# Performance work log

Hardware: AMD Instinct MI355X
Metric: run time of the kernel (lower is better)

Reference implementation:

```python
import jax, jax.numpy as jnp
import numpy as np

HIDDEN = 1024
FFN = 3584
NUM_EXPERTS = 8
TOP_K = 2
B, S = 2, 1024


def setup_inputs() -> dict:
    key = jax.random.key(0)
    k0, k1, k2, k3 = jax.random.split(key, 4)
    hidden_states = jax.random.normal(k0, (B, S, HIDDEN), dtype=jnp.float32)
    # torch Linear stores [out, in]; we keep gate as [E, H] (matches nn.Linear weight)
    gate_w = jax.random.normal(k1, (NUM_EXPERTS, HIDDEN), dtype=jnp.float32) * 0.02
    # GroupedLinear weights stored as [E, in, out] for direct x @ W per expert
    w_gate_up = jax.random.normal(k2, (NUM_EXPERTS, HIDDEN, 2 * FFN), dtype=jnp.float32) * 0.02
    w_down = jax.random.normal(k3, (NUM_EXPERTS, FFN, HIDDEN), dtype=jnp.float32) * 0.02
    return {"hidden_states": hidden_states, "gate_w": gate_w,
            "w_gate_up": w_gate_up, "w_down": w_down}


def reference(hidden_states, gate_w, w_gate_up, w_down):
    b, s, h = hidden_states.shape
    x = hidden_states.reshape(-1, h)                      # [T, H]
    T = x.shape[0]
    E = gate_w.shape[0]

    # Router: logits -> fp32 softmax -> top-k -> renormalize (Mixtral semantics)
    router_logits = x @ gate_w.T                          # [T, E]
    probs = jax.nn.softmax(router_logits.astype(jnp.float32), axis=-1)
    top_vals, top_idx = jax.lax.top_k(probs, TOP_K)       # [T, K]
    top_vals = top_vals / top_vals.sum(axis=-1, keepdims=True)
    top_vals = top_vals.astype(x.dtype)

    # Dense combine weights [T, E]: scatter top-k probs to expert slots.
    # Equivalent to permute -> grouped GEMM -> unpermute-with-probs.
    combine = jnp.zeros((T, E), dtype=x.dtype).at[
        jnp.arange(T)[:, None], top_idx].add(top_vals)

    out = jnp.zeros_like(x)
    for e in range(E):  # fixed small expert count
        gu = x @ w_gate_up[e]                             # [T, 2F]
        gate_proj, up_proj = jnp.split(gu, 2, axis=-1)
        act = jax.nn.silu(gate_proj) * up_proj            # [T, F]
        out = out + combine[:, e:e + 1] * (act @ w_down[e])

    return out.reshape(b, s, h), router_logits
```

## Files before the change

### kernel.cpp

```cpp
#include <hip/hip_runtime.h>
#include <hip/hip_bf16.h>
#include <stdint.h>

#define HIDDEN  1024
#define FFN     3584
#define NE      8
#define NTOK    2048
#define CAP     2048
#define OUT_ELEMS (NTOK * HIDDEN)

#define X_OFF   0u
#define CNT_OFF (4u*1024u*1024u)
#define TOK_OFF (CNT_OFF + 256u)
#define WGT_OFF (TOK_OFF + 65536u)
#define ACT_OFF (WGT_OFF + 65536u)

typedef __attribute__((ext_vector_type(8))) short short8;
typedef __attribute__((ext_vector_type(4))) float floatx4;

static __device__ __forceinline__ uint32_t f2bf(float f) {
  union { float f; uint32_t u; } v; v.f = f;
  return (v.u + 0x7FFFu + ((v.u >> 16) & 1u)) >> 16;
}
static __device__ __forceinline__ uint32_t pack2(float lo, float hi) {
  return f2bf(lo) | (f2bf(hi) << 16);
}
union S8U { uint4 u; short8 s; };
static __device__ __forceinline__ short8 as_short8(uint4 v) { S8U x; x.u = v; return x.s; }

__global__ __launch_bounds__(256) void moe_prep(float4* __restrict__ out4,
                                                int* __restrict__ cnt) {
  uint32_t i = blockIdx.x * 256u + threadIdx.x;
  out4[i] = make_float4(0.f, 0.f, 0.f, 0.f);
  if (blockIdx.x == 0 && threadIdx.x < NE) cnt[threadIdx.x] = 0;
}

__global__ __launch_bounds__(256) void moe_convert(const float4* __restrict__ x4,
                                                   uint4* __restrict__ xb) {
  uint32_t g = blockIdx.x * 256u + threadIdx.x;
  float4 a = x4[2u*g], b = x4[2u*g + 1u];
  xb[g] = make_uint4(pack2(a.x, a.y), pack2(a.z, a.w),
                     pack2(b.x, b.y), pack2(b.z, b.w));
}

__global__ __launch_bounds__(256) void moe_router(
    const float* __restrict__ x, const float* __restrict__ gw,
    float* __restrict__ logits, int* __restrict__ cnt,
    int* __restrict__ tok, float* __restrict__ wgt)
{
  const int t = blockIdx.x * 4 + (threadIdx.x >> 6);
  const int lane = threadIdx.x & 63;
  const float* xr = x + (size_t)t * HIDDEN;
  float a[NE];
#pragma unroll
  for (int e = 0; e < NE; ++e) a[e] = 0.f;
  for (int hh = 0; hh < HIDDEN / 64; ++hh) {
    float xv = xr[hh * 64 + lane];
#pragma unroll
    for (int e = 0; e < NE; ++e) a[e] += xv * gw[e * HIDDEN + hh * 64 + lane];
  }
#pragma unroll
  for (int off = 32; off > 0; off >>= 1) {
#pragma unroll
    for (int e = 0; e < NE; ++e) a[e] += __shfl_xor(a[e], off);
  }
  if (lane == 0) {
#pragma unroll
    for (int e = 0; e < NE; ++e) logits[t * NE + e] = a[e];
    int i0 = 0; float v0 = a[0];
#pragma unroll
    for (int e = 1; e < NE; ++e) if (a[e] > v0) { v0 = a[e]; i0 = e; }
    int i1 = (i0 == 0) ? 1 : 0; float v1 = a[i1];
#pragma unroll
    for (int e = 0; e < NE; ++e) if (e != i0 && a[e] > v1) { v1 = a[e]; i1 = e; }
    float w0 = 1.f / (1.f + __expf(v1 - v0));
    float w1 = 1.f - w0;
    int p0 = atomicAdd(&cnt[i0], 1); tok[i0 * CAP + p0] = t; wgt[i0 * CAP + p0] = w0;
    int p1 = atomicAdd(&cnt[i1], 1); tok[i1 * CAP + p1] = t; wgt[i1 * CAP + p1] = w1;
  }
}

__global__ __launch_bounds__(256) void moe_gateup(
    const uint4* __restrict__ xb, const float* __restrict__ wgu,
    const int* __restrict__ cnt, const int* __restrict__ tok,
    unsigned short* __restrict__ act)
{
  const int e  = blockIdx.z;
  const int m0 = blockIdx.y * 128;
  const int f0 = blockIdx.x * 64;
  const int cn = cnt[e];
  if (m0 >= cn) return;
  int basev = 0;
#pragma unroll
  for (int i = 0; i < NE; ++i) { int ci = cnt[i]; if (i < e) basev += ci; }

  __shared__ uint4    As[1024];
  __shared__ uint32_t Bs[4096];

  const int tid  = threadIdx.x;
  const int lane = tid & 63;
  const int w    = tid >> 6;
  const int wm   = w >> 1, wn = w & 1;
  const int q    = lane >> 4;
  const int c    = lane & 15;

  floatx4 acc[4][4];
#pragma unroll
  for (int i = 0; i < 4; ++i)
#pragma unroll
    for (int j = 0; j < 4; ++j) acc[i][j] = (floatx4){0.f, 0.f, 0.f, 0.f};

  const float* wB  = wgu + (size_t)e * HIDDEN * (2 * FFN);
  const int* tokE  = tok + e * CAP;

  for (int kt = 0; kt < HIDDEN / 64; ++kt) {
    const int k0 = kt * 64;
    __syncthreads();
#pragma unroll
    for (int it = 0; it < 4; ++it) {
      int cid = it * 256 + tid;
      int row = cid >> 3, c8 = cid & 7;
      int mrow = m0 + row; if (mrow >= cn) mrow = cn - 1;
      int tk = tokE[mrow];
      As[row * 8 + (c8 ^ (row & 7))] = xb[(size_t)tk * (HIDDEN / 8) + (k0 >> 3) + c8];
    }
#pragma unroll
    for (int it = 0; it < 4; ++it) {
      int mid = it * 256 + tid;
      int kp = mid >> 5;
      int n  = (mid & 31) * 4;
      int col = f0 + ((n >> 6) << 5) + (n & 31) + (((n >> 5) & 1) ? FFN : 0);
      const float* src = wB + (size_t)(k0 + 2 * kp) * (2 * FFN) + col;
      float4 r0 = *(const float4*)src;
      float4 r1 = *(const float4*)(src + 2 * FFN);
      int widx = kp * 128 + (n ^ (((kp >> 2) & 1) << 4));
      *(uint4*)&Bs[widx] = make_uint4(pack2(r0.x, r1.x), pack2(r0.y, r1.y),
                                      pack2(r0.z, r1.z), pack2(r0.w, r1.w));
    }
    __syncthreads();
#pragma unroll
    for (int ks = 0; ks < 2; ++ks) {
      short8 af[4];
#pragma unroll
      for (int i = 0; i < 4; ++i) {
        int row = wm * 64 + i * 16 + c;
        int kc8 = ks * 4 + q;
        af[i] = as_short8(As[row * 8 + (kc8 ^ (row & 7))]);
      }
      short8 bfr[4];
#pragma unroll
      for (int j = 0; j < 4; ++j) {
        int n  = wn * 64 + j * 16 + c;
        int kp = ks * 16 + q * 4;
        int nn = n ^ ((q & 1) << 4);
        bfr[j] = as_short8(make_uint4(Bs[(kp + 0) * 128 + nn], Bs[(kp + 1) * 128 + nn],
                                      Bs[(kp + 2) * 128 + nn], Bs[(kp + 3) * 128 + nn]));
      }
#pragma unroll
      for (int i = 0; i < 4; ++i)
#pragma unroll
        for (int j = 0; j < 4; ++j)
          acc[i][j] = __builtin_amdgcn_mfma_f32_16x16x32_bf16(af[i], bfr[j], acc[i][j], 0, 0, 0);
    }
  }

#pragma unroll
  for (int i = 0; i < 4; ++i) {
#pragma unroll
    for (int r = 0; r < 4; ++r) {
      int m = m0 + wm * 64 + i * 16 + q * 4 + r;
      if (m < cn) {
#pragma unroll
        for (int j = 0; j < 2; ++j) {
          float g = acc[i][j][r];
          float u = acc[i][j + 2][r];
          float a = (g / (1.f + __expf(-g))) * u;
          act[(size_t)(basev + m) * FFN + (f0 + wn * 32 + j * 16 + c)] = (unsigned short)f2bf(a);
        }
      }
    }
  }
}

__global__ __launch_bounds__(256) void moe_down(
    const uint4* __restrict__ actc, const float* __restrict__ wd,
    const int* __restrict__ cnt, const int* __restrict__ tok,
    const float* __restrict__ wgt, float* __restrict__ out)
{
  const int e  = blockIdx.z;
  const int m0 = blockIdx.y * 128;
  const int n0 = blockIdx.x * 128;
  const int cn = cnt[e];
  if (m0 >= cn) return;
  int basev = 0;
#pragma unroll
  for (int i = 0; i < NE; ++i) { int ci = cnt[i]; if (i < e) basev += ci; }

  __shared__ uint4    As[1024];
  __shared__ uint32_t Bs[4096];

  const int tid  = threadIdx.x;
  const int lane = tid & 63;
  const int w    = tid >> 6;
  const int wm   = w >> 1, wn = w & 1;
  const int q    = lane >> 4;
  const int c    = lane & 15;

  floatx4 acc[4][4];
#pragma unroll
  for (int i = 0; i < 4; ++i)
#pragma unroll
    for (int j = 0; j < 4; ++j) acc[i][j] = (floatx4){0.f, 0.f, 0.f, 0.f};

  const float* wB = wd + (size_t)e * FFN * HIDDEN;

  for (int kt = 0; kt < FFN / 64; ++kt) {
    const int k0 = kt * 64;
    __syncthreads();
#pragma unroll
    for (int it = 0; it < 4; ++it) {
      int cid = it * 256 + tid;
      int row = cid >> 3, c8 = cid & 7;
      int mrow = m0 + row; if (mrow >= cn) mrow = cn - 1;
      As[row * 8 + (c8 ^ (row & 7))] =
          actc[(size_t)(basev + mrow) * (FFN / 8) + (k0 >> 3) + c8];
    }
#pragma unroll
    for (int it = 0; it < 4; ++it) {
      int mid = it * 256 + tid;
      int kp = mid >> 5;
      int n  = (mid & 31) * 4;
      int col = n0 + n;
      const float* src = wB + (size_t)(k0 + 2 * kp) * HIDDEN + col;
      float4 r0 = *(const float4*)src;
      float4 r1 = *(const float4*)(src + HIDDEN);
      int widx = kp * 128 + (n ^ (((kp >> 2) & 1) << 4));
      *(uint4*)&Bs[widx] = make_uint4(pack2(r0.x, r1.x), pack2(r0.y, r1.y),
                                      pack2(r0.z, r1.z), pack2(r0.w, r1.w));
    }
    __syncthreads();
#pragma unroll
    for (int ks = 0; ks < 2; ++ks) {
      short8 af[4];
#pragma unroll
      for (int i = 0; i < 4; ++i) {
        int row = wm * 64 + i * 16 + c;
        int kc8 = ks * 4 + q;
        af[i] = as_short8(As[row * 8 + (kc8 ^ (row & 7))]);
      }
      short8 bfr[4];
#pragma unroll
      for (int j = 0; j < 4; ++j) {
        int n  = wn * 64 + j * 16 + c;
        int kp = ks * 16 + q * 4;
        int nn = n ^ ((q & 1) << 4);
        bfr[j] = as_short8(make_uint4(Bs[(kp + 0) * 128 + nn], Bs[(kp + 1) * 128 + nn],
                                      Bs[(kp + 2) * 128 + nn], Bs[(kp + 3) * 128 + nn]));
      }
#pragma unroll
      for (int i = 0; i < 4; ++i)
#pragma unroll
        for (int j = 0; j < 4; ++j)
          acc[i][j] = __builtin_amdgcn_mfma_f32_16x16x32_bf16(af[i], bfr[j], acc[i][j], 0, 0, 0);
    }
  }

#pragma unroll
  for (int i = 0; i < 4; ++i) {
#pragma unroll
    for (int r = 0; r < 4; ++r) {
      int m = m0 + wm * 64 + i * 16 + q * 4 + r;
      if (m < cn) {
        int   t  = tok[e * CAP + m];
        float wg = wgt[e * CAP + m];
        float* orow = out + (size_t)t * HIDDEN + n0 + wn * 64 + c;
#pragma unroll
        for (int j = 0; j < 4; ++j)
          atomicAdd(orow + j * 16, acc[i][j][r] * wg);
      }
    }
  }
}

extern "C" void kernel_launch(void* const* d_in, const int* in_sizes, int n_in,
                              void* d_out, int out_size, void* d_ws, size_t ws_size,
                              hipStream_t stream)
{
  (void)in_sizes; (void)n_in; (void)out_size; (void)ws_size;
  const float* x   = (const float*)d_in[0];
  const float* gw  = (const float*)d_in[1];
  const float* wgu = (const float*)d_in[2];
  const float* wd  = (const float*)d_in[3];
  float* out = (float*)d_out;
  char*  ws  = (char*)d_ws;

  uint4*          xb  = (uint4*)(ws + X_OFF);
  int*            cnt = (int*)(ws + CNT_OFF);
  int*            tok = (int*)(ws + TOK_OFF);
  float*          wgt = (float*)(ws + WGT_OFF);
  unsigned short* act = (unsigned short*)(ws + ACT_OFF);

  moe_prep<<<OUT_ELEMS / (256 * 4), 256, 0, stream>>>((float4*)out, cnt);
  moe_convert<<<(NTOK * HIDDEN) / (256 * 8), 256, 0, stream>>>((const float4*)x, xb);
  moe_router<<<NTOK / 4, 256, 0, stream>>>(x, gw, out + OUT_ELEMS, cnt, tok, wgt);
  moe_gateup<<<dim3(FFN / 64, 16, NE), 256, 0, stream>>>(xb, wgu, cnt, tok, act);
  moe_down<<<dim3(HIDDEN / 128, 16, NE), 256, 0, stream>>>((const uint4*)act, wd, cnt, tok, wgt, out);
}
```

Baseline: 630.8 us.

## Fuse bf16 convert into router, retile expert GEMMs with tall M tiles and split-K down

The separate x-to-bf16 conversion kernel is folded into the router, which now reads x as float4 and computes logits from registers. Both expert GEMMs switch to 512-thread blocks with 512-row M tiles and narrow 32/64-column N tiles over K=32 steps. The fp32 weight tiles are register-prefetched one step ahead and stored in small padded LDS buffers. The down projection is split four ways along K, with partial sums combined through the existing atomics. The aim is to stream each weight byte fewer times per expert and add more blocks to the down GEMM, at the cost of smaller K steps, more syncs per FLOP and more output atomics.

```diff
diff --git a/kernel.cpp b/kernel.cpp
--- a/kernel.cpp
+++ b/kernel.cpp
@@ -4,6 +4,7 @@
 
 #define HIDDEN  1024
 #define FFN     3584
+#define FFN2    7168
 #define NE      8
 #define NTOK    2048
 #define CAP     2048
@@ -35,29 +36,29 @@
   if (blockIdx.x == 0 && threadIdx.x < NE) cnt[threadIdx.x] = 0;
 }
 
-__global__ __launch_bounds__(256) void moe_convert(const float4* __restrict__ x4,
-                                                   uint4* __restrict__ xb) {
-  uint32_t g = blockIdx.x * 256u + threadIdx.x;
-  float4 a = x4[2u*g], b = x4[2u*g + 1u];
-  xb[g] = make_uint4(pack2(a.x, a.y), pack2(a.z, a.w),
-                     pack2(b.x, b.y), pack2(b.z, b.w));
-}
-
 __global__ __launch_bounds__(256) void moe_router(
-    const float* __restrict__ x, const float* __restrict__ gw,
+    const float4* __restrict__ x4, const float* __restrict__ gw,
     float* __restrict__ logits, int* __restrict__ cnt,
-    int* __restrict__ tok, float* __restrict__ wgt)
-{
-  const int t = blockIdx.x * 4 + (threadIdx.x >> 6);
+    int* __restrict__ tok, float* __restrict__ wgt, uint4* __restrict__ xb)
+{
+  const int w    = threadIdx.x >> 6;
   const int lane = threadIdx.x & 63;
-  const float* xr = x + (size_t)t * HIDDEN;
+  const int t    = blockIdx.x * 4 + w;
+  const float4* xr = x4 + (size_t)t * 256 + lane * 4;
+  float4 v0 = xr[0], v1 = xr[1], v2 = xr[2], v3 = xr[3];
+  xb[(size_t)t * 128 + lane * 2 + 0] =
+      make_uint4(pack2(v0.x, v0.y), pack2(v0.z, v0.w), pack2(v1.x, v1.y), pack2(v1.z, v1.w));
+  xb[(size_t)t * 128 + lane * 2 + 1] =
+      make_uint4(pack2(v2.x, v2.y), pack2(v2.z, v2.w), pack2(v3.x, v3.y), pack2(v3.z, v3.w));
   float a[NE];
 #pragma unroll
-  for (int e = 0; e < NE; ++e) a[e] = 0.f;
-  for (int hh = 0; hh < HIDDEN / 64; ++hh) {
-    float xv = xr[hh * 64 + lane];
-#pragma unroll
-    for (int e = 0; e < NE; ++e) a[e] += xv * gw[e * HIDDEN + hh * 64 + lane];
+  for (int e = 0; e < NE; ++e) {
+    const float4* g4 = (const float4*)(gw + e * HIDDEN) + lane * 4;
+    float4 g0 = g4[0], g1 = g4[1], g2 = g4[2], g3 = g4[3];
+    a[e] = v0.x*g0.x + v0.y*g0.y + v0.z*g0.z + v0.w*g0.w
+         + v1.x*g1.x + v1.y*g1.y + v1.z*g1.z + v1.w*g1.w
+         + v2.x*g2.x + v2.y*g2.y + v2.z*g2.z + v2.w*g2.w
+         + v3.x*g3.x + v3.y*g3.y + v3.z*g3.z + v3.w*g3.w;
   }
 #pragma unroll
   for (int off = 32; off > 0; off >>= 1) {
@@ -67,145 +68,147 @@
   if (lane == 0) {
 #pragma unroll
     for (int e = 0; e < NE; ++e) logits[t * NE + e] = a[e];
-    int i0 = 0; float v0 = a[0];
-#pragma unroll
-    for (int e = 1; e < NE; ++e) if (a[e] > v0) { v0 = a[e]; i0 = e; }
-    int i1 = (i0 == 0) ? 1 : 0; float v1 = a[i1];
-#pragma unroll
-    for (int e = 0; e < NE; ++e) if (e != i0 && a[e] > v1) { v1 = a[e]; i1 = e; }
-    float w0 = 1.f / (1.f + __expf(v1 - v0));
+    int i0 = 0; float v0s = a[0];
+#pragma unroll
+    for (int e = 1; e < NE; ++e) if (a[e] > v0s) { v0s = a[e]; i0 = e; }
+    int i1 = (i0 == 0) ? 1 : 0; float v1s = a[i1];
+#pragma unroll
+    for (int e = 0; e < NE; ++e) if (e != i0 && a[e] > v1s) { v1s = a[e]; i1 = e; }
+    float w0 = 1.f / (1.f + __expf(v1s - v0s));
     float w1 = 1.f - w0;
     int p0 = atomicAdd(&cnt[i0], 1); tok[i0 * CAP + p0] = t; wgt[i0 * CAP + p0] = w0;
     int p1 = atomicAdd(&cnt[i1], 1); tok[i1 * CAP + p1] = t; wgt[i1 * CAP + p1] = w1;
   }
 }
 
-__global__ __launch_bounds__(256) void moe_gateup(
+__global__ __launch_bounds__(512) void moe_gateup(
     const uint4* __restrict__ xb, const float* __restrict__ wgu,
     const int* __restrict__ cnt, const int* __restrict__ tok,
     unsigned short* __restrict__ act)
 {
   const int e  = blockIdx.z;
-  const int m0 = blockIdx.y * 128;
-  const int f0 = blockIdx.x * 64;
+  const int m0 = blockIdx.y * 512;
+  const int f0 = blockIdx.x * 32;
   const int cn = cnt[e];
   if (m0 >= cn) return;
   int basev = 0;
 #pragma unroll
   for (int i = 0; i < NE; ++i) { int ci = cnt[i]; if (i < e) basev += ci; }
 
-  __shared__ uint4    As[1024];
-  __shared__ uint32_t Bs[4096];
+  __shared__ uint4    As[512 * 5];
+  __shared__ uint32_t Bs[16 * 66];
 
   const int tid  = threadIdx.x;
   const int lane = tid & 63;
   const int w    = tid >> 6;
-  const int wm   = w >> 1, wn = w & 1;
   const int q    = lane >> 4;
   const int c    = lane & 15;
 
+  int aoff[4], alds[4];
+#pragma unroll
+  for (int it = 0; it < 4; ++it) {
+    int cid = it * 512 + tid;
+    int row = cid >> 2, c8 = cid & 3;
+    int mrow = m0 + row; if (mrow >= cn) mrow = cn - 1;
+    int tk = tok[e * CAP + mrow];
+    aoff[it] = tk * 128 + c8;
+    alds[it] = row * 5 + c8;
+  }
+
   floatx4 acc[4][4];
 #pragma unroll
   for (int i = 0; i < 4; ++i)
 #pragma unroll
     for (int j = 0; j < 4; ++j) acc[i][j] = (floatx4){0.f, 0.f, 0.f, 0.f};
 
-  const float* wB  = wgu + (size_t)e * HIDDEN * (2 * FFN);
-  const int* tokE  = tok + e * CAP;
-
-  for (int kt = 0; kt < HIDDEN / 64; ++kt) {
-    const int k0 = kt * 64;
-    __syncthreads();
-#pragma unroll
-    for (int it = 0; it < 4; ++it) {
-      int cid = it * 256 + tid;
-      int row = cid >> 3, c8 = cid & 7;
-      int mrow = m0 + row; if (mrow >= cn) mrow = cn - 1;
-      int tk = tokE[mrow];
-      As[row * 8 + (c8 ^ (row & 7))] = xb[(size_t)tk * (HIDDEN / 8) + (k0 >> 3) + c8];
-    }
-#pragma unroll
-    for (int it = 0; it < 4; ++it) {
-      int mid = it * 256 + tid;
-      int kp = mid >> 5;
-      int n  = (mid & 31) * 4;
-      int col = f0 + ((n >> 6) << 5) + (n & 31) + (((n >> 5) & 1) ? FFN : 0);
-      const float* src = wB + (size_t)(k0 + 2 * kp) * (2 * FFN) + col;
-      float4 r0 = *(const float4*)src;
-      float4 r1 = *(const float4*)(src + 2 * FFN);
-      int widx = kp * 128 + (n ^ (((kp >> 2) & 1) << 4));
-      *(uint4*)&Bs[widx] = make_uint4(pack2(r0.x, r1.x), pack2(r0.y, r1.y),
-                                      pack2(r0.z, r1.z), pack2(r0.w, r1.w));
-    }
-    __syncthreads();
-#pragma unroll
-    for (int ks = 0; ks < 2; ++ks) {
-      short8 af[4];
-#pragma unroll
-      for (int i = 0; i < 4; ++i) {
-        int row = wm * 64 + i * 16 + c;
-        int kc8 = ks * 4 + q;
-        af[i] = as_short8(As[row * 8 + (kc8 ^ (row & 7))]);
-      }
-      short8 bfr[4];
-#pragma unroll
-      for (int j = 0; j < 4; ++j) {
-        int n  = wn * 64 + j * 16 + c;
-        int kp = ks * 16 + q * 4;
-        int nn = n ^ ((q & 1) << 4);
-        bfr[j] = as_short8(make_uint4(Bs[(kp + 0) * 128 + nn], Bs[(kp + 1) * 128 + nn],
-                                      Bs[(kp + 2) * 128 + nn], Bs[(kp + 3) * 128 + nn]));
-      }
-#pragma unroll
-      for (int i = 0; i < 4; ++i)
-#pragma unroll
-        for (int j = 0; j < 4; ++j)
-          acc[i][j] = __builtin_amdgcn_mfma_f32_16x16x32_bf16(af[i], bfr[j], acc[i][j], 0, 0, 0);
-    }
+  const float* wB = wgu + (size_t)e * HIDDEN * FFN2;
+  const int kp = tid >> 5;
+  const int n2 = (tid & 31) * 2;
+  const int bcol = (n2 < 32) ? (f0 + n2) : (FFN + f0 + (n2 - 32));
+  const float* bsrc = wB + (size_t)(2 * kp) * FFN2 + bcol;
+  float2 r0 = *(const float2*)(bsrc);
+  float2 r1 = *(const float2*)(bsrc + FFN2);
+
+  for (int kt = 0; kt < 32; ++kt) {
+    __syncthreads();
+    *(uint2*)&Bs[kp * 66 + n2] = make_uint2(pack2(r0.x, r1.x), pack2(r0.y, r1.y));
+#pragma unroll
+    for (int it = 0; it < 4; ++it) As[alds[it]] = xb[aoff[it] + kt * 4];
+    __syncthreads();
+    int kn = (kt + 1 < 32) ? (kt + 1) : 31;
+    const float* nb = bsrc + (size_t)kn * 32 * FFN2;
+    r0 = *(const float2*)(nb);
+    r1 = *(const float2*)(nb + FFN2);
+
+    short8 af[4];
+#pragma unroll
+    for (int i = 0; i < 4; ++i) af[i] = as_short8(As[(w * 64 + i * 16 + c) * 5 + q]);
+    short8 bfr[4];
+#pragma unroll
+    for (int j = 0; j < 4; ++j) {
+      int b0 = (q * 4) * 66 + j * 16 + c;
+      bfr[j] = as_short8(make_uint4(Bs[b0], Bs[b0 + 66], Bs[b0 + 132], Bs[b0 + 198]));
+    }
+#pragma unroll
+    for (int i = 0; i < 4; ++i)
+#pragma unroll
+      for (int j = 0; j < 4; ++j)
+        acc[i][j] = __builtin_amdgcn_mfma_f32_16x16x32_bf16(af[i], bfr[j], acc[i][j], 0, 0, 0);
   }
 
 #pragma unroll
   for (int i = 0; i < 4; ++i) {
 #pragma unroll
     for (int r = 0; r < 4; ++r) {
-      int m = m0 + wm * 64 + i * 16 + q * 4 + r;
+      int m = m0 + w * 64 + i * 16 + q * 4 + r;
       if (m < cn) {
 #pragma unroll
         for (int j = 0; j < 2; ++j) {
           float g = acc[i][j][r];
           float u = acc[i][j + 2][r];
           float a = (g / (1.f + __expf(-g))) * u;
-          act[(size_t)(basev + m) * FFN + (f0 + wn * 32 + j * 16 + c)] = (unsigned short)f2bf(a);
+          act[(size_t)(basev + m) * FFN + (f0 + j * 16 + c)] = (unsigned short)f2bf(a);
         }
       }
     }
   }
 }
 
-__global__ __launch_bounds__(256) void moe_down(
+__global__ __launch_bounds__(512) void moe_down(
     const uint4* __restrict__ actc, const float* __restrict__ wd,
     const int* __restrict__ cnt, const int* __restrict__ tok,
     const float* __restrict__ wgt, float* __restrict__ out)
 {
-  const int e  = blockIdx.z;
-  const int m0 = blockIdx.y * 128;
-  const int n0 = blockIdx.x * 128;
+  const int bz = blockIdx.z;
+  const int e  = bz >> 2;
+  const int sl = bz & 3;
+  const int m0 = blockIdx.y * 512;
+  const int n0 = blockIdx.x * 64;
   const int cn = cnt[e];
   if (m0 >= cn) return;
   int basev = 0;
 #pragma unroll
   for (int i = 0; i < NE; ++i) { int ci = cnt[i]; if (i < e) basev += ci; }
 
-  __shared__ uint4    As[1024];
-  __shared__ uint32_t Bs[4096];
+  __shared__ uint4    As[512 * 5];
+  __shared__ uint32_t Bs[16 * 66];
 
   const int tid  = threadIdx.x;
   const int lane = tid & 63;
   const int w    = tid >> 6;
-  const int wm   = w >> 1, wn = w & 1;
   const int q    = lane >> 4;
   const int c    = lane & 15;
 
+  int aoff[4], alds[4];
+#pragma unroll
+  for (int it = 0; it < 4; ++it) {
+    int cid = it * 512 + tid;
+    int row = cid >> 2, c8 = cid & 3;
+    int mrow = m0 + row; if (mrow >= cn) mrow = cn - 1;
+    aoff[it] = (basev + mrow) * 448 + sl * 112 + c8;
+    alds[it] = row * 5 + c8;
+  }
+
   floatx4 acc[4][4];
 #pragma unroll
   for (int i = 0; i < 4; ++i)
@@ -213,67 +216,49 @@
     for (int j = 0; j < 4; ++j) acc[i][j] = (floatx4){0.f, 0.f, 0.f, 0.f};
 
   const float* wB = wd + (size_t)e * FFN * HIDDEN;
-
-  for (int kt = 0; kt < FFN / 64; ++kt) {
-    const int k0 = kt * 64;
-    __syncthreads();
-#pragma unroll
-    for (int it = 0; it < 4; ++it) {
-      int cid = it * 256 + tid;
-      int row = cid >> 3, c8 = cid & 7;
-      int mrow = m0 + row; if (mrow >= cn) mrow = cn - 1;
-      As[row * 8 + (c8 ^ (row & 7))] =
-          actc[(size_t)(basev + mrow) * (FFN / 8) + (k0 >> 3) + c8];
-    }
-#pragma unroll
-    for (int it = 0; it < 4; ++it) {
-      int mid = it * 256 + tid;
-      int kp = mid >> 5;
-      int n  = (mid & 31) * 4;
-      int col = n0 + n;
-      const float* src = wB + (size_t)(k0 + 2 * kp) * HIDDEN + col;
-      float4 r0 = *(const float4*)src;
-      float4 r1 = *(const float4*)(src + HIDDEN);
-      int widx = kp * 128 + (n ^ (((kp >> 2) & 1) << 4));
-      *(uint4*)&Bs[widx] = make_uint4(pack2(r0.x, r1.x), pack2(r0.y, r1.y),
-                                      pack2(r0.z, r1.z), pack2(r0.w, r1.w));
-    }
-    __syncthreads();
-#pragma unroll
-    for (int ks = 0; ks < 2; ++ks) {
-      short8 af[4];
-#pragma unroll
-      for (int i = 0; i < 4; ++i) {
-        int row = wm * 64 + i * 16 + c;
-        int kc8 = ks * 4 + q;
-        af[i] = as_short8(As[row * 8 + (kc8 ^ (row & 7))]);
-      }
-      short8 bfr[4];
-#pragma unroll
-      for (int j = 0; j < 4; ++j) {
-        int n  = wn * 64 + j * 16 + c;
-        int kp = ks * 16 + q * 4;
-        int nn = n ^ ((q & 1) << 4);
-        bfr[j] = as_short8(make_uint4(Bs[(kp + 0) * 128 + nn], Bs[(kp + 1) * 128 + nn],
-                                      Bs[(kp + 2) * 128 + nn], Bs[(kp + 3) * 128 + nn]));
-      }
-#pragma unroll
-      for (int i = 0; i < 4; ++i)
-#pragma unroll
-        for (int j = 0; j < 4; ++j)
-          acc[i][j] = __builtin_amdgcn_mfma_f32_16x16x32_bf16(af[i], bfr[j], acc[i][j], 0, 0, 0);
-    }
+  const int kp = tid >> 5;
+  const int n2 = (tid & 31) * 2;
+  const int col = n0 + n2;
+  const float* bsrc = wB + (size_t)(sl * 896 + 2 * kp) * HIDDEN + col;
+  float2 r0 = *(const float2*)(bsrc);
+  float2 r1 = *(const float2*)(bsrc + HIDDEN);
+
+  for (int kt = 0; kt < 28; ++kt) {
+    __syncthreads();
+    *(uint2*)&Bs[kp * 66 + n2] = make_uint2(pack2(r0.x, r1.x), pack2(r0.y, r1.y));
+#pragma unroll
+    for (int it = 0; it < 4; ++it) As[alds[it]] = actc[aoff[it] + kt * 4];
+    __syncthreads();
+    int kn = (kt + 1 < 28) ? (kt + 1) : 27;
+    const float* nb = bsrc + (size_t)kn * 32 * HIDDEN;
+    r0 = *(const float2*)(nb);
+    r1 = *(const float2*)(nb + HIDDEN);
+
+    short8 af[4];
+#pragma unroll
+    for (int i = 0; i < 4; ++i) af[i] = as_short8(As[(w * 64 + i * 16 + c) * 5 + q]);
+    short8 bfr[4];
+#pragma unroll
+    for (int j = 0; j < 4; ++j) {
+      int b0 = (q * 4) * 66 + j * 16 + c;
+      bfr[j] = as_short8(make_uint4(Bs[b0], Bs[b0 + 66], Bs[b0 + 132], Bs[b0 + 198]));
+    }
+#pragma unroll
+    for (int i = 0; i < 4; ++i)
+#pragma unroll
+      for (int j = 0; j < 4; ++j)
+        acc[i][j] = __builtin_amdgcn_mfma_f32_16x16x32_bf16(af[i], bfr[j], acc[i][j], 0, 0, 0);
   }
 
 #pragma unroll
   for (int i = 0; i < 4; ++i) {
 #pragma unroll
     for (int r = 0; r < 4; ++r) {
-      int m = m0 + wm * 64 + i * 16 + q * 4 + r;
+      int m = m0 + w * 64 + i * 16 + q * 4 + r;
       if (m < cn) {
         int   t  = tok[e * CAP + m];
         float wg = wgt[e * CAP + m];
-        float* orow = out + (size_t)t * HIDDEN + n0 + wn * 64 + c;
+        float* orow = out + (size_t)t * HIDDEN + n0 + c;
 #pragma unroll
         for (int j = 0; j < 4; ++j)
           atomicAdd(orow + j * 16, acc[i][j][r] * wg);
@@ -301,8 +286,9 @@
   unsigned short* act = (unsigned short*)(ws + ACT_OFF);
 
   moe_prep<<<OUT_ELEMS / (256 * 4), 256, 0, stream>>>((float4*)out, cnt);
-  moe_convert<<<(NTOK * HIDDEN) / (256 * 8), 256, 0, stream>>>((const float4*)x, xb);
-  moe_router<<<NTOK / 4, 256, 0, stream>>>(x, gw, out + OUT_ELEMS, cnt, tok, wgt);
-  moe_gateup<<<dim3(FFN / 64, 16, NE), 256, 0, stream>>>(xb, wgu, cnt, tok, act);
-  moe_down<<<dim3(HIDDEN / 128, 16, NE), 256, 0, stream>>>((const uint4*)act, wd, cnt, tok, wgt, out);
-}
+  moe_router<<<NTOK / 4, 256, 0, stream>>>((const float4*)x, gw, out + OUT_ELEMS,
+                                           cnt, tok, wgt, xb);
+  moe_gateup<<<dim3(FFN / 32, 4, NE), 512, 0, stream>>>(xb, wgu, cnt, tok, act);
+  moe_down<<<dim3(HIDDEN / 64, 4, NE * 4), 512, 0, stream>>>((const uint4*)act, wd,
+                                                             cnt, tok, wgt, out);
+}
```

Result: slower. 721.7 us (+14.4%).
